# Performance work log

Hardware: AMD Instinct MI355X
Metric: run time of the kernel (lower is better)

## Reference

```python
import jax, jax.numpy as jnp
import numpy as np

MAX_SEQ = 2048
NUM_HEADS = 32
NUM_KV_HEADS = 4
HEAD_DIM = 256
HIDDEN = 4096
ROTARY_DIM = 64  # head_dim * partial_rotary_factor(0.25)
THETA = 10000000.0
EPS = 1e-6
GROUPS = NUM_HEADS // NUM_KV_HEADS
SCALE = 1.0 / np.sqrt(HEAD_DIM)


def rms_norm(x, w):
    xf = x.astype(jnp.float32)
    norm = jax.lax.rsqrt(jnp.mean(xf * xf, axis=-1, keepdims=True) + EPS)
    return (xf * norm * w).astype(x.dtype)


def partial_rope(x, position):
    # x: [B, H, 1, D]; rotate first ROTARY_DIM dims (split-half convention)
    half = ROTARY_DIM // 2
    inv_freq = 1.0 / (THETA ** (jnp.arange(half, dtype=jnp.float32) / half))
    freqs = position.astype(jnp.float32) * inv_freq  # [half]
    cos = jnp.cos(freqs).reshape(1, 1, 1, -1)
    sin = jnp.sin(freqs).reshape(1, 1, 1, -1)
    x1 = x[..., :half]
    x2 = x[..., half:ROTARY_DIM]
    x_pass = x[..., ROTARY_DIM:]
    rot = jnp.concatenate([x1 * cos - x2 * sin, x2 * cos + x1 * sin], axis=-1)
    return jnp.concatenate([rot, x_pass], axis=-1)


def setup_inputs() -> dict:
    key = jax.random.key(0)
    ks = jax.random.split(key, 10)
    pos = 1500
    position = jnp.array([pos], dtype=jnp.int32)
    idx = jnp.arange(MAX_SEQ)
    mask = jnp.where(idx <= pos, 0.0, -1e9).astype(jnp.float32).reshape(1, 1, 1, MAX_SEQ)
    onehot = (idx == pos).astype(jnp.float32).reshape(1, 1, MAX_SEQ, 1)
    return {
        "x": jax.random.normal(ks[0], (1, 1, HIDDEN), dtype=jnp.float32),
        "position": position,
        "mask": mask,
        "k_cache": jax.random.normal(ks[1], (1, NUM_KV_HEADS, MAX_SEQ, HEAD_DIM), dtype=jnp.float32),
        "v_cache": jax.random.normal(ks[2], (1, NUM_KV_HEADS, MAX_SEQ, HEAD_DIM), dtype=jnp.float32),
        "onehot": onehot,
        "q_proj_w": jax.random.normal(ks[3], (2 * NUM_HEADS * HEAD_DIM, HIDDEN), dtype=jnp.float32) * 0.02,
        "k_proj_w": jax.random.normal(ks[4], (NUM_KV_HEADS * HEAD_DIM, HIDDEN), dtype=jnp.float32) * 0.02,
        "v_proj_w": jax.random.normal(ks[5], (NUM_KV_HEADS * HEAD_DIM, HIDDEN), dtype=jnp.float32) * 0.02,
        "o_proj_w": jax.random.normal(ks[6], (HIDDEN, NUM_HEADS * HEAD_DIM), dtype=jnp.float32) * 0.02,
        "q_norm_w": jnp.ones((HEAD_DIM,), dtype=jnp.float32),
        "k_norm_w": jnp.ones((HEAD_DIM,), dtype=jnp.float32),
    }


def reference(x, position, mask, k_cache, v_cache, onehot,
              q_proj_w, k_proj_w, v_proj_w, o_proj_w, q_norm_w, k_norm_w):
    B, T, _ = x.shape  # B=T=1
    # Q + gate interleaved per head
    qg = jnp.einsum('bth,oh->bto', x, q_proj_w).reshape(B, T, NUM_HEADS, 2 * HEAD_DIM)
    q = qg[..., :HEAD_DIM]                      # [B,T,H,D]
    gate = qg[..., HEAD_DIM:].reshape(B, T, -1)  # [B,T,H*D]
    q = jnp.transpose(q, (0, 2, 1, 3))           # [B,H,T,D]
    k = jnp.einsum('bth,oh->bto', x, k_proj_w).reshape(B, T, NUM_KV_HEADS, HEAD_DIM).transpose(0, 2, 1, 3)
    v = jnp.einsum('bth,oh->bto', x, v_proj_w).reshape(B, T, NUM_KV_HEADS, HEAD_DIM).transpose(0, 2, 1, 3)
    q = rms_norm(q, q_norm_w)
    k = rms_norm(k, k_norm_w)
    q = partial_rope(q, position)
    k = partial_rope(k, position)
    # full-buffer onehot cache update (same math as mul_/add_)
    k_cache = k_cache * (1.0 - onehot) + k * onehot  # [B,KV,S,D]
    v_cache = v_cache * (1.0 - onehot) + v * onehot
    # GQA: group query heads over kv heads without materializing expanded KV
    qg_heads = q.reshape(B, NUM_KV_HEADS, GROUPS, T, HEAD_DIM)
    attn = jnp.einsum('bgktd,bgsd->bgkts', qg_heads, k_cache) * SCALE  # [B,KV,G,T,S]
    attn = attn + mask[:, :, None]  # mask [B,1,1,T,S] broadcast
    attn = jax.nn.softmax(attn, axis=-1)
    out = jnp.einsum('bgkts,bgsd->bgktd', attn, v_cache)  # [B,KV,G,T,D]
    out = out.reshape(B, NUM_HEADS, T, HEAD_DIM).transpose(0, 2, 1, 3).reshape(B, T, -1)
    out = out * jax.nn.sigmoid(gate)
    return jnp.einsum('bto,ho->bth', out, o_proj_w)
```

## Files before the change

kernel.cpp:

```cpp
#include <hip/hip_runtime.h>
#include <math.h>

#define MAX_SEQ   2048
#define NUM_HEADS 32
#define NUM_KV    4
#define HEAD_DIM  256
#define HIDDEN    4096
#define ROT_DIM   64
#define GROUPS    8
#define SCALE     0.0625f
#define CHUNK     32
#define NCHUNK    (MAX_SEQ / CHUNK)

typedef float f4 __attribute__((ext_vector_type(4)));

__device__ inline f4 ntload4(const float* p) {
    return __builtin_nontemporal_load(reinterpret_cast<const f4*>(p));
}

__global__ __launch_bounds__(256) void gemv_qkv(
    const float* __restrict__ x,
    const float* __restrict__ qw,
    const float* __restrict__ kw,
    const float* __restrict__ vw,
    float* __restrict__ out)
{
    const int row = blockIdx.x;
    const int tid = threadIdx.x;

    const float* w;
    if (row < 16384)      w = qw + (size_t)row * HIDDEN;
    else if (row < 17408) w = kw + (size_t)(row - 16384) * HIDDEN;
    else                  w = vw + (size_t)(row - 17408) * HIDDEN;

    float acc = 0.f;
#pragma unroll
    for (int j = 0; j < 4; ++j) {
        const int col = j * 1024 + tid * 4;
        f4 wv = ntload4(w + col);
        f4 xv = *reinterpret_cast<const f4*>(x + col);
        acc += wv[0] * xv[0] + wv[1] * xv[1] + wv[2] * xv[2] + wv[3] * xv[3];
    }
#pragma unroll
    for (int off = 32; off >= 1; off >>= 1) acc += __shfl_xor(acc, off);
    __shared__ float red[4];
    if ((tid & 63) == 0) red[tid >> 6] = acc;
    __syncthreads();
    if (tid == 0) out[row] = red[0] + red[1] + red[2] + red[3];
}

__global__ __launch_bounds__(256) void attn_partial(
    const float* __restrict__ qkv,
    const float* __restrict__ qnw,
    const float* __restrict__ knw,
    const float* __restrict__ kcache,
    const float* __restrict__ vcache,
    const int*   __restrict__ posp,
    float* __restrict__ part_m,
    float* __restrict__ part_l,
    float* __restrict__ part_acc)
{
    const int kv  = blockIdx.x;
    const int c   = blockIdx.y;
    const int pos = posp[0];
    const int s0  = c * CHUNK;
    const int tid = threadIdx.x;

    if (s0 > pos) {
        if (tid == 0) {
#pragma unroll
            for (int g = 0; g < GROUPS; ++g) {
                const int pid = (kv * GROUPS + g) * NCHUNK + c;
                part_m[pid] = -1e30f; part_l[pid] = 0.f;
            }
        }
        return;
    }
    const int s1 = min(s0 + CHUNK, pos + 1);

    const int lane = tid & 63;
    const int wave = tid >> 6;
    const int d    = tid;

    float vals[9];
#pragma unroll
    for (int g = 0; g < GROUPS; ++g)
        vals[g] = qkv[(kv * GROUPS + g) * 512 + d];
    vals[8] = qkv[16384 + kv * HEAD_DIM + d];

    __shared__ float ssred[9][4];
    {
        float sq[9];
#pragma unroll
        for (int g = 0; g < 9; ++g) sq[g] = vals[g] * vals[g];
#pragma unroll
        for (int off = 32; off >= 1; off >>= 1) {
#pragma unroll
            for (int g = 0; g < 9; ++g) sq[g] += __shfl_xor(sq[g], off);
        }
        if (lane == 0) {
#pragma unroll
            for (int g = 0; g < 9; ++g) ssred[g][wave] = sq[g];
        }
    }
    __syncthreads();

    __shared__ __align__(16) float qn[9][HEAD_DIM];
    {
        const float qw_ = qnw[d];
        const float kw_ = knw[d];
#pragma unroll
        for (int g = 0; g < 9; ++g) {
            const float tot  = ssred[g][0] + ssred[g][1] + ssred[g][2] + ssred[g][3];
            const float norm = rsqrtf(tot * (1.0f / HEAD_DIM) + 1e-6f);
            qn[g][d] = vals[g] * norm * (g < 8 ? qw_ : kw_);
        }
    }
    __syncthreads();

    if (d < ROT_DIM) {
        const int i = d & 31;
        const double inv_freq = pow(10000000.0, -(double)i / 32.0);
        const double ang = (double)pos * inv_freq;
        const float co = (float)cos(ang);
        const float si = (float)sin(ang);
        float rv[9];
#pragma unroll
        for (int g = 0; g < 9; ++g) {
            const float x1 = qn[g][i];
            const float x2 = qn[g][i + 32];
            rv[g] = (d < 32) ? (x1 * co - x2 * si) : (x2 * co + x1 * si);
        }
        __syncthreads();
#pragma unroll
        for (int g = 0; g < 9; ++g) qn[g][d] = rv[g];
    } else {
        __syncthreads();
    }
    __syncthreads();

    const float* kbase = kcache + (size_t)kv * MAX_SEQ * HEAD_DIM;
    const float* vbase = vcache + (size_t)kv * MAX_SEQ * HEAD_DIM;

    f4 q8[GROUPS];
#pragma unroll
    for (int g = 0; g < GROUPS; ++g)
        q8[g] = *reinterpret_cast<const f4*>(&qn[g][lane * 4]);

    __shared__ float sc[GROUPS][CHUNK];
    __shared__ float pl[GROUPS][CHUNK];
    __shared__ float mh[GROUPS], lh[GROUPS];

    for (int i = wave; i < CHUNK; i += 4) {
        const int s = s0 + i;
        float part[GROUPS];
#pragma unroll
        for (int g = 0; g < GROUPS; ++g) part[g] = 0.f;
        const bool valid = (s < s1);
        if (valid) {
            f4 kvec;
            if (s == pos) kvec = *reinterpret_cast<const f4*>(&qn[8][lane * 4]);
            else          kvec = ntload4(kbase + (size_t)s * HEAD_DIM + lane * 4);
#pragma unroll
            for (int g = 0; g < GROUPS; ++g) {
                f4 t = q8[g] * kvec;
                part[g] += t[0] + t[1] + t[2] + t[3];
            }
        }
#pragma unroll
        for (int off = 32; off >= 1; off >>= 1) {
#pragma unroll
            for (int g = 0; g < GROUPS; ++g)
                part[g] += __shfl_xor(part[g], off);
        }
        if (lane == 0) {
#pragma unroll
            for (int g = 0; g < GROUPS; ++g)
                sc[g][i] = valid ? part[g] * SCALE : -1e30f;
        }
    }
    __syncthreads();

    {
        const int h = tid >> 5;
        const int j = tid & 31;
        float v = sc[h][j];
        float m = v;
#pragma unroll
        for (int off = 16; off >= 1; off >>= 1)
            m = fmaxf(m, __shfl_xor(m, off));
        const float p = expf(v - m);
        pl[h][j] = p;
        float ls = p;
#pragma unroll
        for (int off = 16; off >= 1; off >>= 1)
            ls += __shfl_xor(ls, off);
        if (j == 0) { mh[h] = m; lh[h] = ls; }
    }
    __syncthreads();

    float acc[GROUPS];
#pragma unroll
    for (int g = 0; g < GROUPS; ++g) acc[g] = 0.f;
    const float* vnew = qkv + 17408 + kv * HEAD_DIM;
    for (int s = s0; s < s1; ++s) {
        const float v = (s == pos) ? vnew[d]
                                   : __builtin_nontemporal_load(vbase + (size_t)s * HEAD_DIM + d);
        const int i = s - s0;
#pragma unroll
        for (int g = 0; g < GROUPS; ++g) acc[g] += pl[g][i] * v;
    }
#pragma unroll
    for (int g = 0; g < GROUPS; ++g) {
        const int pid = (kv * GROUPS + g) * NCHUNK + c;
        part_acc[(size_t)pid * HEAD_DIM + d] = acc[g];
        if (tid == 0) { part_m[pid] = mh[g]; part_l[pid] = lh[g]; }
    }
}

__global__ __launch_bounds__(256) void attn_combine(
    const float* __restrict__ part_m,
    const float* __restrict__ part_l,
    const float* __restrict__ part_acc,
    const float* __restrict__ qkv,
    float* __restrict__ attn_gated)
{
    const int h = blockIdx.x;
    const int d = threadIdx.x;

    float M = -1e30f;
    for (int c = 0; c < NCHUNK; ++c) M = fmaxf(M, part_m[h * NCHUNK + c]);

    float L = 0.f, acc = 0.f;
    for (int c = 0; c < NCHUNK; ++c) {
        const float lc = part_l[h * NCHUNK + c];
        if (lc > 0.f) {
            const float w = expf(part_m[h * NCHUNK + c] - M);
            L   += lc * w;
            acc += part_acc[(size_t)(h * NCHUNK + c) * HEAD_DIM + d] * w;
        }
    }
    const float o   = acc / L;
    const float g   = qkv[h * 512 + 256 + d];
    const float sig = 1.0f / (1.0f + expf(-g));
    attn_gated[h * HEAD_DIM + d] = o * sig;
}

__global__ __launch_bounds__(256) void gemv_o(
    const float* __restrict__ vec,
    const float* __restrict__ w,
    float* __restrict__ out)
{
    const int row = blockIdx.x;
    const int tid = threadIdx.x;
    const float* wr = w + (size_t)row * 8192;

    float acc = 0.f;
#pragma unroll
    for (int j = 0; j < 8; ++j) {
        const int col = j * 1024 + tid * 4;
        f4 wv = ntload4(wr + col);
        f4 xv = *reinterpret_cast<const f4*>(vec + col);
        acc += wv[0] * xv[0] + wv[1] * xv[1] + wv[2] * xv[2] + wv[3] * xv[3];
    }
#pragma unroll
    for (int off = 32; off >= 1; off >>= 1) acc += __shfl_xor(acc, off);
    __shared__ float red[4];
    if ((tid & 63) == 0) red[tid >> 6] = acc;
    __syncthreads();
    if (tid == 0) out[row] = red[0] + red[1] + red[2] + red[3];
}

extern "C" void kernel_launch(void* const* d_in, const int* in_sizes, int n_in,
                              void* d_out, int out_size, void* d_ws, size_t ws_size,
                              hipStream_t stream) {
    const float* x        = (const float*)d_in[0];
    const int*   position = (const int*)  d_in[1];
    const float* k_cache  = (const float*)d_in[3];
    const float* v_cache  = (const float*)d_in[4];
    const float* q_proj_w = (const float*)d_in[6];
    const float* k_proj_w = (const float*)d_in[7];
    const float* v_proj_w = (const float*)d_in[8];
    const float* o_proj_w = (const float*)d_in[9];
    const float* q_norm_w = (const float*)d_in[10];
    const float* k_norm_w = (const float*)d_in[11];
    float* out = (float*)d_out;

    float* ws         = (float*)d_ws;
    float* qkv        = ws;
    float* part_m     = ws + 18432;
    float* part_l     = ws + 20480;
    float* part_acc   = ws + 22528;
    float* attn_gated = ws + 546816;

    gemv_qkv<<<18432, 256, 0, stream>>>(x, q_proj_w, k_proj_w, v_proj_w, qkv);
    dim3 g2(NUM_KV, NCHUNK);
    attn_partial<<<g2, 256, 0, stream>>>(qkv, q_norm_w, k_norm_w,
                                         k_cache, v_cache, position,
                                         part_m, part_l, part_acc);
    attn_combine<<<NUM_HEADS, 256, 0, stream>>>(part_m, part_l, part_acc, qkv,
                                                attn_gated);
    gemv_o<<<4096, 256, 0, stream>>>(attn_gated, o_proj_w, out);
}
```

Baseline: 113.0 us.

## Use one wave per GEMV row, precompute RoPE table, batch KV loads

The QKV and O projection GEMVs now give each wave its own weight row, which removes the shared-memory block reduction and barrier and cuts the block count by four. A tiny extra kernel precomputes the RoPE cos/sin table once in double precision, so attention blocks no longer call pow/cos/sin. In attention, each wave issues all eight of its K-row loads before computing, and the V loop is unrolled by four with vectorised probability reads, to raise memory-level parallelism. The cost is one extra kernel launch. Per-thread register use also rises.

After: 108.0 us. 1.05x faster.

```diff
diff --git a/kernel.cpp b/kernel.cpp
--- a/kernel.cpp
+++ b/kernel.cpp
@@ -18,6 +18,16 @@
     return __builtin_nontemporal_load(reinterpret_cast<const f4*>(p));
 }
 
+__global__ void rope_table(const int* __restrict__ posp, float* __restrict__ tab) {
+    const int i = threadIdx.x;
+    if (i < 32) {
+        const double inv_freq = pow(10000000.0, -(double)i / 32.0);
+        const double ang = (double)posp[0] * inv_freq;
+        tab[i]      = (float)cos(ang);
+        tab[i + 32] = (float)sin(ang);
+    }
+}
+
 __global__ __launch_bounds__(256) void gemv_qkv(
     const float* __restrict__ x,
     const float* __restrict__ qw,
@@ -25,8 +35,9 @@
     const float* __restrict__ vw,
     float* __restrict__ out)
 {
-    const int row = blockIdx.x;
-    const int tid = threadIdx.x;
+    const int wave = threadIdx.x >> 6;
+    const int lane = threadIdx.x & 63;
+    const int row  = blockIdx.x * 4 + wave;
 
     const float* w;
     if (row < 16384)      w = qw + (size_t)row * HIDDEN;
@@ -35,18 +46,15 @@
 
     float acc = 0.f;
 #pragma unroll
-    for (int j = 0; j < 4; ++j) {
-        const int col = j * 1024 + tid * 4;
-        f4 wv = ntload4(w + col);
-        f4 xv = *reinterpret_cast<const f4*>(x + col);
+    for (int it = 0; it < HIDDEN / 256; ++it) {
+        const int idx = it * 256 + lane * 4;
+        f4 wv = ntload4(w + idx);
+        f4 xv = *reinterpret_cast<const f4*>(x + idx);
         acc += wv[0] * xv[0] + wv[1] * xv[1] + wv[2] * xv[2] + wv[3] * xv[3];
     }
 #pragma unroll
     for (int off = 32; off >= 1; off >>= 1) acc += __shfl_xor(acc, off);
-    __shared__ float red[4];
-    if ((tid & 63) == 0) red[tid >> 6] = acc;
-    __syncthreads();
-    if (tid == 0) out[row] = red[0] + red[1] + red[2] + red[3];
+    if (lane == 0) out[row] = acc;
 }
 
 __global__ __launch_bounds__(256) void attn_partial(
@@ -55,6 +63,7 @@
     const float* __restrict__ knw,
     const float* __restrict__ kcache,
     const float* __restrict__ vcache,
+    const float* __restrict__ tab,
     const int*   __restrict__ posp,
     float* __restrict__ part_m,
     float* __restrict__ part_l,
@@ -118,12 +127,11 @@
     }
     __syncthreads();
 
-    if (d < ROT_DIM) {
-        const int i = d & 31;
-        const double inv_freq = pow(10000000.0, -(double)i / 32.0);
-        const double ang = (double)pos * inv_freq;
-        const float co = (float)cos(ang);
-        const float si = (float)sin(ang);
+    {
+        const bool rot = (d < ROT_DIM);
+        const int  i   = d & 31;
+        const float co = tab[i];
+        const float si = tab[i + 32];
         float rv[9];
 #pragma unroll
         for (int g = 0; g < 9; ++g) {
@@ -132,12 +140,12 @@
             rv[g] = (d < 32) ? (x1 * co - x2 * si) : (x2 * co + x1 * si);
         }
         __syncthreads();
-#pragma unroll
-        for (int g = 0; g < 9; ++g) qn[g][d] = rv[g];
-    } else {
+        if (rot) {
+#pragma unroll
+            for (int g = 0; g < 9; ++g) qn[g][d] = rv[g];
+        }
         __syncthreads();
     }
-    __syncthreads();
 
     const float* kbase = kcache + (size_t)kv * MAX_SEQ * HEAD_DIM;
     const float* vbase = vcache + (size_t)kv * MAX_SEQ * HEAD_DIM;
@@ -148,35 +156,39 @@
         q8[g] = *reinterpret_cast<const f4*>(&qn[g][lane * 4]);
 
     __shared__ float sc[GROUPS][CHUNK];
-    __shared__ float pl[GROUPS][CHUNK];
+    __shared__ __align__(16) float pl[GROUPS][CHUNK];
     __shared__ float mh[GROUPS], lh[GROUPS];
 
-    for (int i = wave; i < CHUNK; i += 4) {
-        const int s = s0 + i;
-        float part[GROUPS];
-#pragma unroll
-        for (int g = 0; g < GROUPS; ++g) part[g] = 0.f;
-        const bool valid = (s < s1);
-        if (valid) {
-            f4 kvec;
-            if (s == pos) kvec = *reinterpret_cast<const f4*>(&qn[8][lane * 4]);
-            else          kvec = ntload4(kbase + (size_t)s * HEAD_DIM + lane * 4);
+    {
+        const int i0 = wave * 8;
+        f4 kvec[8];
+#pragma unroll
+        for (int j = 0; j < 8; ++j) {
+            const int s = s0 + i0 + j;
+            if (s < pos) kvec[j] = ntload4(kbase + (size_t)s * HEAD_DIM + lane * 4);
+            else         kvec[j] = *reinterpret_cast<const f4*>(&qn[8][lane * 4]);
+        }
+#pragma unroll
+        for (int j = 0; j < 8; ++j) {
+            const int s = s0 + i0 + j;
+            const bool valid = (s < s1);
+            float part[GROUPS];
 #pragma unroll
             for (int g = 0; g < GROUPS; ++g) {
-                f4 t = q8[g] * kvec;
-                part[g] += t[0] + t[1] + t[2] + t[3];
+                f4 t = q8[g] * kvec[j];
+                part[g] = t[0] + t[1] + t[2] + t[3];
             }
-        }
-#pragma unroll
-        for (int off = 32; off >= 1; off >>= 1) {
-#pragma unroll
-            for (int g = 0; g < GROUPS; ++g)
-                part[g] += __shfl_xor(part[g], off);
-        }
-        if (lane == 0) {
-#pragma unroll
-            for (int g = 0; g < GROUPS; ++g)
-                sc[g][i] = valid ? part[g] * SCALE : -1e30f;
+#pragma unroll
+            for (int off = 32; off >= 1; off >>= 1) {
+#pragma unroll
+                for (int g = 0; g < GROUPS; ++g)
+                    part[g] += __shfl_xor(part[g], off);
+            }
+            if (lane == 0) {
+#pragma unroll
+                for (int g = 0; g < GROUPS; ++g)
+                    sc[g][i0 + j] = valid ? part[g] * SCALE : -1e30f;
+            }
         }
     }
     __syncthreads();
@@ -203,12 +215,25 @@
 #pragma unroll
     for (int g = 0; g < GROUPS; ++g) acc[g] = 0.f;
     const float* vnew = qkv + 17408 + kv * HEAD_DIM;
-    for (int s = s0; s < s1; ++s) {
-        const float v = (s == pos) ? vnew[d]
-                                   : __builtin_nontemporal_load(vbase + (size_t)s * HEAD_DIM + d);
-        const int i = s - s0;
-#pragma unroll
-        for (int g = 0; g < GROUPS; ++g) acc[g] += pl[g][i] * v;
+#pragma unroll
+    for (int i4 = 0; i4 < CHUNK / 4; ++i4) {
+        float vv[4];
+#pragma unroll
+        for (int u = 0; u < 4; ++u) {
+            const int s = s0 + i4 * 4 + u;
+            vv[u] = (s < pos) ? __builtin_nontemporal_load(vbase + (size_t)s * HEAD_DIM + d)
+                              : vnew[d];
+        }
+        f4 p4[GROUPS];
+#pragma unroll
+        for (int g = 0; g < GROUPS; ++g)
+            p4[g] = *reinterpret_cast<const f4*>(&pl[g][i4 * 4]);
+#pragma unroll
+        for (int u = 0; u < 4; ++u) {
+#pragma unroll
+            for (int g = 0; g < GROUPS; ++g)
+                acc[g] += p4[g][u] * vv[u];
+        }
     }
 #pragma unroll
     for (int g = 0; g < GROUPS; ++g) {
@@ -251,24 +276,22 @@
     const float* __restrict__ w,
     float* __restrict__ out)
 {
-    const int row = blockIdx.x;
-    const int tid = threadIdx.x;
+    const int wave = threadIdx.x >> 6;
+    const int lane = threadIdx.x & 63;
+    const int row  = blockIdx.x * 4 + wave;
     const float* wr = w + (size_t)row * 8192;
 
     float acc = 0.f;
 #pragma unroll
-    for (int j = 0; j < 8; ++j) {
-        const int col = j * 1024 + tid * 4;
-        f4 wv = ntload4(wr + col);
-        f4 xv = *reinterpret_cast<const f4*>(vec + col);
+    for (int it = 0; it < 8192 / 256; ++it) {
+        const int idx = it * 256 + lane * 4;
+        f4 wv = ntload4(wr + idx);
+        f4 xv = *reinterpret_cast<const f4*>(vec + idx);
         acc += wv[0] * xv[0] + wv[1] * xv[1] + wv[2] * xv[2] + wv[3] * xv[3];
     }
 #pragma unroll
     for (int off = 32; off >= 1; off >>= 1) acc += __shfl_xor(acc, off);
-    __shared__ float red[4];
-    if ((tid & 63) == 0) red[tid >> 6] = acc;
-    __syncthreads();
-    if (tid == 0) out[row] = red[0] + red[1] + red[2] + red[3];
+    if (lane == 0) out[row] = acc;
 }
 
 extern "C" void kernel_launch(void* const* d_in, const int* in_sizes, int n_in,
@@ -288,17 +311,19 @@
 
     float* ws         = (float*)d_ws;
     float* qkv        = ws;
-    float* part_m     = ws + 18432;
-    float* part_l     = ws + 20480;
-    float* part_acc   = ws + 22528;
-    float* attn_gated = ws + 546816;
-
-    gemv_qkv<<<18432, 256, 0, stream>>>(x, q_proj_w, k_proj_w, v_proj_w, qkv);
+    float* tab        = ws + 18432;
+    float* part_m     = ws + 18496;
+    float* part_l     = ws + 20544;
+    float* part_acc   = ws + 22592;
+    float* attn_gated = ws + 546880;
+
+    rope_table<<<1, 64, 0, stream>>>(position, tab);
+    gemv_qkv<<<18432 / 4, 256, 0, stream>>>(x, q_proj_w, k_proj_w, v_proj_w, qkv);
     dim3 g2(NUM_KV, NCHUNK);
     attn_partial<<<g2, 256, 0, stream>>>(qkv, q_norm_w, k_norm_w,
-                                         k_cache, v_cache, position,
+                                         k_cache, v_cache, tab, position,
                                          part_m, part_l, part_acc);
     attn_combine<<<NUM_HEADS, 256, 0, stream>>>(part_m, part_l, part_acc, qkv,
                                                 attn_gated);
-    gemv_o<<<4096, 256, 0, stream>>>(attn_gated, o_proj_w, out);
-}
+    gemv_o<<<4096 / 4, 256, 0, stream>>>(attn_gated, o_proj_w, out);
+}
```
